# Kernel optimization log

Hardware: AMD Instinct MI355X
Metric: run time of the kernel (lower is better)

## Reference

```python
import jax, jax.numpy as jnp
import numpy as np

B, S, D, H, DFF = 4, 2048, 768, 12, 3072
DK = D // H

def setup_inputs() -> dict:
    key = jax.random.key(0)
    ks = jax.random.split(key, 16)
    sc = 0.02
    inp = {
        'src': jax.random.normal(ks[0], (B, S, D), jnp.float32),
        'mask': jnp.ones((B, 1, 1, S), jnp.int32),
        'Wq': jax.random.normal(ks[1], (D, D), jnp.float32) * sc,
        'bq': jnp.zeros((D,), jnp.float32),
        'Wk': jax.random.normal(ks[2], (D, D), jnp.float32) * sc,
        'bk': jnp.zeros((D,), jnp.float32),
        'Wv': jax.random.normal(ks[3], (D, D), jnp.float32) * sc,
        'bv': jnp.zeros((D,), jnp.float32),
        'Wo': jax.random.normal(ks[4], (D, D), jnp.float32) * sc,
        'bo': jnp.zeros((D,), jnp.float32),
        'W1': jax.random.normal(ks[5], (D, DFF), jnp.float32) * sc,
        'b1': jnp.zeros((DFF,), jnp.float32),
        'W2': jax.random.normal(ks[6], (DFF, D), jnp.float32) * sc,
        'b2': jnp.zeros((D,), jnp.float32),
        'ln1_g': jnp.ones((D,), jnp.float32), 'ln1_b': jnp.zeros((D,), jnp.float32),
        'ln2_g': jnp.ones((D,), jnp.float32), 'ln2_b': jnp.zeros((D,), jnp.float32),
    }
    return inp

def _layernorm(x, g, b, eps=1e-5):
    mu = jnp.mean(x, axis=-1, keepdims=True)
    var = jnp.mean(jnp.square(x - mu), axis=-1, keepdims=True)
    return (x - mu) * jax.lax.rsqrt(var + eps) * g + b

def reference(src, mask, Wq, bq, Wk, bk, Wv, bv, Wo, bo, W1, b1, W2, b2, ln1_g, ln1_b, ln2_g, ln2_b):
    # Multi-head self-attention (dropout in eval mode -> identity)
    q = (src @ Wq + bq).reshape(B, S, H, DK).transpose(0, 2, 1, 3)  # [B,H,S,dk]
    k = (src @ Wk + bk).reshape(B, S, H, DK).transpose(0, 2, 1, 3)
    v = (src @ Wv + bv).reshape(B, S, H, DK).transpose(0, 2, 1, 3)
    scores = jnp.einsum('bhqd,bhkd->bhqk', q, k) / jnp.sqrt(jnp.float32(DK))
    scores = jnp.where(mask == 0, jnp.float32(-1e9), scores)
    attn = jax.nn.softmax(scores, axis=-1)
    ctx = jnp.einsum('bhqk,bhkd->bhqd', attn, v)  # [B,H,S,dk]
    ctx = ctx.transpose(0, 2, 1, 3).reshape(B, S, D)
    attn_out = ctx @ Wo + bo
    x = _layernorm(src + attn_out, ln1_g, ln1_b)
    ffn = jax.nn.relu(x @ W1 + b1) @ W2 + b2
    return _layernorm(x + ffn, ln2_g, ln2_b)
```

## Files before the change

kernel.cpp:

```cpp
#include <hip/hip_runtime.h>
#include <hip/hip_bf16.h>
#include <stdint.h>

constexpr int BB = 4;
constexpr int SS = 2048;
constexpr int DD = 768;
constexpr int HH = 12;
constexpr int DKK = 64;
constexpr int DFF2 = 3072;
constexpr int MR = BB * SS;

typedef __attribute__((ext_vector_type(4))) short short4v;
typedef __attribute__((ext_vector_type(8))) short short8v;
typedef __attribute__((ext_vector_type(4))) float f32x4;
typedef __attribute__((ext_vector_type(16))) float f32x16;
typedef __attribute__((ext_vector_type(4))) float float4v;
typedef __attribute__((ext_vector_type(4))) unsigned int u32x4;

static __device__ inline short f2bs(float f) {
    __hip_bfloat16 h = __float2bfloat16(f);
    return (short)__builtin_bit_cast(unsigned short, h);
}
static __device__ inline float bs2f(short s) {
    __hip_bfloat16 h = __builtin_bit_cast(__hip_bfloat16, (unsigned short)s);
    return __bfloat162float(h);
}

static __device__ inline void glds16(const void* g, void* l) {
    __builtin_amdgcn_global_load_lds(
        (const __attribute__((address_space(1))) void*)g,
        (__attribute__((address_space(3))) void*)l, 16, 0, 0);
}

static __device__ inline unsigned cvtpk(float a, float b) {
    unsigned d;
    asm("v_cvt_pk_bf16_f32 %0, %1, %2" : "=v"(d) : "v"(a), "v"(b));
    return d;
}
static __device__ inline short8v pk4(unsigned a, unsigned b, unsigned c, unsigned d) {
    u32x4 w; w[0] = a; w[1] = b; w[2] = c; w[3] = d;
    return __builtin_bit_cast(short8v, w);
}

static __device__ inline void bar_vmcnt4() {
    __builtin_amdgcn_sched_barrier(0);
    asm volatile("s_waitcnt vmcnt(4)" ::: "memory");
    __builtin_amdgcn_s_barrier();
    __builtin_amdgcn_sched_barrier(0);
}
static __device__ inline void bar_vmcnt0() {
    __builtin_amdgcn_sched_barrier(0);
    asm volatile("s_waitcnt vmcnt(0)" ::: "memory");
    __builtin_amdgcn_s_barrier();
    __builtin_amdgcn_sched_barrier(0);
}

__global__ __launch_bounds__(256) void cast_f32_bf16(const float* __restrict__ in,
                                                     short* __restrict__ out, int n) {
    int i = (blockIdx.x * 256 + threadIdx.x) * 4;
    if (i < n) {
        float4v v = *(const float4v*)&in[i];
        short4v o;
        o[0] = f2bs(v[0]); o[1] = f2bs(v[1]); o[2] = f2bs(v[2]); o[3] = f2bs(v[3]);
        *(short4v*)&out[i] = o;
    }
}

__global__ __launch_bounds__(256) void transpose_cast(const float* __restrict__ W,
                                                      short* __restrict__ Wt, int K, int N) {
    __shared__ float tile[32][33];
    int n0 = blockIdx.x * 32, k0 = blockIdx.y * 32;
    int tx = threadIdx.x & 31, ty = threadIdx.x >> 5;
    #pragma unroll
    for (int i = 0; i < 32; i += 8)
        tile[ty + i][tx] = W[(size_t)(k0 + ty + i) * N + n0 + tx];
    __syncthreads();
    #pragma unroll
    for (int i = 0; i < 32; i += 8)
        Wt[(size_t)(n0 + ty + i) * K + k0 + tx] = f2bs(tile[tx][ty + i]);
}

__global__ __launch_bounds__(256) void vtrans(const short* __restrict__ V,
                                              short* __restrict__ Vt) {
    __shared__ short t[64][72];
    const int tid = threadIdx.x;
    const size_t base = (size_t)blockIdx.y * SS * DKK;
    const int s0 = blockIdx.x * 64;
    int r = tid >> 3, c = (tid & 7) * 8;
    #pragma unroll
    for (int it = 0; it < 2; it++)
        *(short8v*)&t[it * 32 + r][c] =
            *(const short8v*)&V[base + (size_t)(s0 + it * 32 + r) * DKK + c];
    __syncthreads();
    int d = tid >> 2, grp = (tid & 3) * 16;
    short8v o0, o1;
    #pragma unroll
    for (int e = 0; e < 8; e++) {
        int p0 = e, p1 = 8 + e;
        o0[e] = t[grp + (p0 & 3) + 8 * ((p0 >> 2) & 1) + 4 * (p0 >> 3)][d];
        o1[e] = t[grp + (p1 & 3) + 8 * ((p1 >> 2) & 1) + 4 * (p1 >> 3)][d];
    }
    int c0 = 2 * (tid & 3), c1 = c0 + 1;
    int p0 = c0 ^ (d & 7), p1 = c1 ^ (d & 7);
    *(short8v*)&Vt[base + (size_t)d * SS + s0 + p0 * 8] = o0;
    *(short8v*)&Vt[base + (size_t)d * SS + s0 + p1 * 8] = o1;
}

template <int EPI>
__global__ __launch_bounds__(256) void gemm_bt(
    const short* __restrict__ A, const short* __restrict__ Bt,
    int Nn, int Kn,
    const float* __restrict__ bias0, const float* __restrict__ bias1,
    const float* __restrict__ bias2,
    short* __restrict__ out0, short* __restrict__ out1, short* __restrict__ out2) {
    __shared__ alignas(16) short sA[3][128 * 32];
    __shared__ alignas(16) short sB[3][128 * 32];
    const int tid = threadIdx.x;
    const int wave = tid >> 6, lane = tid & 63;
    const int g = lane >> 4, qq = lane & 15;
    const int wm = (wave >> 1) * 64, wn = (wave & 1) * 64;

    const int gx = gridDim.x;
    const int nwg = gx * gridDim.y;
    const int wgid = blockIdx.y * gx + blockIdx.x;
    const int cpx = nwg >> 3;
    const int swz = (wgid & 7) * cpx + (wgid >> 3);
    const int bx = swz % gx, by = swz / gx;
    const int m0 = by * 128, n0 = bx * 128;

    const int e0 = wave * 512 + lane * 8;
    const int r0 = e0 >> 5, c0 = e0 & 31;

    const f32x4 zero = {0.0f, 0.0f, 0.0f, 0.0f};
    f32x4 acc[4][4];
    #pragma unroll
    for (int i = 0; i < 4; i++)
        #pragma unroll
        for (int j = 0; j < 4; j++) acc[i][j] = zero;

    const int NK = Kn >> 5;
    glds16(&A[(size_t)(m0 + r0) * Kn + c0], &sA[0][wave * 512]);
    glds16(&A[(size_t)(m0 + r0 + 64) * Kn + c0], &sA[0][wave * 512 + 2048]);
    glds16(&Bt[(size_t)(n0 + r0) * Kn + c0], &sB[0][wave * 512]);
    glds16(&Bt[(size_t)(n0 + r0 + 64) * Kn + c0], &sB[0][wave * 512 + 2048]);
    __syncthreads();

    int cur = 0, nxt = 1;
    for (int kt = 0; kt < NK; ++kt) {
        if (kt + 1 < NK) {
            const int k1 = (kt + 1) * 32;
            glds16(&A[(size_t)(m0 + r0) * Kn + k1 + c0], &sA[nxt][wave * 512]);
            glds16(&A[(size_t)(m0 + r0 + 64) * Kn + k1 + c0], &sA[nxt][wave * 512 + 2048]);
            glds16(&Bt[(size_t)(n0 + r0) * Kn + k1 + c0], &sB[nxt][wave * 512]);
            glds16(&Bt[(size_t)(n0 + r0 + 64) * Kn + k1 + c0], &sB[nxt][wave * 512 + 2048]);
            bar_vmcnt4();
        } else {
            bar_vmcnt0();
        }
        short8v af[4], bf[4];
        #pragma unroll
        for (int i = 0; i < 4; i++) {
            af[i] = *(const short8v*)&sA[cur][(wm + i * 16 + qq) * 32 + 8 * g];
            bf[i] = *(const short8v*)&sB[cur][(wn + i * 16 + qq) * 32 + 8 * g];
        }
        #pragma unroll
        for (int i = 0; i < 4; i++)
            #pragma unroll
            for (int j = 0; j < 4; j++)
                acc[i][j] = __builtin_amdgcn_mfma_f32_16x16x32_bf16(af[i], bf[j], acc[i][j], 0, 0, 0);
        cur = nxt;
        nxt = (nxt == 2) ? 0 : nxt + 1;
    }

    if (EPI == 2) {
        int which = bx / 6;
        const float* bias = (which == 0) ? bias0 : ((which == 1) ? bias1 : bias2);
        short* outp = (which == 0) ? out0 : ((which == 1) ? out1 : out2);
        float scale = (which == 0) ? 0.125f * 1.44269504088896f : 1.0f;
        #pragma unroll
        for (int i = 0; i < 4; i++)
            #pragma unroll
            for (int j = 0; j < 4; j++)
                #pragma unroll
                for (int r = 0; r < 4; r++) {
                    int row = m0 + wm + i * 16 + g * 4 + r;
                    int col = n0 - which * DD + wn + j * 16 + qq;
                    float vv = (acc[i][j][r] + bias[col]) * scale;
                    int b_ = row >> 11, s_ = row & 2047;
                    int h_ = col >> 6, d_ = col & 63;
                    if (which == 1)
                        d_ = (((d_ >> 3) ^ (s_ & 7)) << 3) | (d_ & 7);
                    outp[(((size_t)(b_ * HH + h_)) * SS + s_) * DKK + d_] = f2bs(vv);
                }
    } else {
        #pragma unroll
        for (int i = 0; i < 4; i++)
            #pragma unroll
            for (int j = 0; j < 4; j++)
                #pragma unroll
                for (int r = 0; r < 4; r++) {
                    int row = m0 + wm + i * 16 + g * 4 + r;
                    int col = n0 + wn + j * 16 + qq;
                    float vv = acc[i][j][r] + bias0[col];
                    if (EPI == 1) vv = fmaxf(vv, 0.0f);
                    out0[(size_t)row * Nn + col] = f2bs(vv);
                }
    }
}

__global__ __launch_bounds__(256) void attn_kernel(
    const short* __restrict__ Q, const short* __restrict__ Kb,
    const short* __restrict__ Vt, const int* __restrict__ mask,
    short* __restrict__ ctx) {
    __shared__ alignas(16) short sK[3][64 * 64];
    __shared__ alignas(16) short sV[3][64 * 64];
    __shared__ unsigned char smask[256];
    const int tid = threadIdx.x;
    const int wave = tid >> 6, lane = tid & 63;
    const int hi = lane >> 5, ln = lane & 31;
    constexpr int NT = SS / 64;

    int flat = blockIdx.y * gridDim.x + blockIdx.x;
    int nw = (flat & 7) * 96 + (flat >> 3);
    const int bh = nw >> 4, qb = nw & 15;
    const int b_ = bh / HH, h_ = bh % HH;
    const int q0 = qb * 128 + wave * 32;
    const size_t base = (size_t)bh * SS * DKK;

    {
        const int* mp = mask + b_ * SS + tid * 8;
        unsigned char by = 0;
        #pragma unroll
        for (int e = 0; e < 8; e++) by |= (unsigned char)((mp[e] != 0) << e);
        smask[tid] = by;
    }

    short8v qf[4];
    {
        const short* qp = &Q[base + (size_t)(q0 + ln) * DKK];
        #pragma unroll
        for (int c = 0; c < 4; c++)
            qf[c] = *(const short8v*)(qp + 16 * c + 8 * hi);
    }

    f32x16 O0, O1, Lacc;
    #pragma unroll
    for (int r = 0; r < 16; r++) { O0[r] = 0.0f; O1[r] = 0.0f; Lacc[r] = 0.0f; }
    f32x16 ZEROV;
    #pragma unroll
    for (int r = 0; r < 16; r++) ZEROV[r] = 0.0f;
    short8v ones8;
    #pragma unroll
    for (int e = 0; e < 8; e++) ones8[e] = (short)0x3F80;

    const int stgrow = wave * 8 + (lane >> 3);
    const int stgc = (lane & 7) * 8;
    const int rsz = (ln & 7) << 4;

    glds16(&Kb[base + (size_t)stgrow * DKK + stgc], &sK[0][wave * 512]);
    glds16(&Kb[base + (size_t)(stgrow + 32) * DKK + stgc], &sK[0][2048 + wave * 512]);
    glds16(&Vt[base + (size_t)stgrow * SS + stgc], &sV[0][wave * 512]);
    glds16(&Vt[base + (size_t)(stgrow + 32) * SS + stgc], &sV[0][2048 + wave * 512]);
    __syncthreads();

    int cur = 0, nxt = 1;
    for (int t = 0; t < NT; ++t) {
        const int kv0 = t * 64;
        if (t + 1 < NT) {
            const int kn = kv0 + 64;
            glds16(&Kb[base + (size_t)(kn + stgrow) * DKK + stgc], &sK[nxt][wave * 512]);
            glds16(&Kb[base + (size_t)(kn + stgrow + 32) * DKK + stgc], &sK[nxt][2048 + wave * 512]);
            glds16(&Vt[base + (size_t)stgrow * SS + kn + stgc], &sV[nxt][wave * 512]);
            glds16(&Vt[base + (size_t)(stgrow + 32) * SS + kn + stgc], &sV[nxt][2048 + wave * 512]);
            bar_vmcnt4();
        } else {
            bar_vmcnt0();
        }
        const char* kr0 = (const char*)&sK[cur][0] + ln * 128;
        const char* kr1 = kr0 + 32 * 128;
        const char* vr0 = (const char*)&sV[cur][0] + ln * 128;
        const char* vr1 = vr0 + 32 * 128;

        f32x16 s0, s1;
        __builtin_amdgcn_s_setprio(1);
        {
            int off = (16 * hi) ^ rsz;
            s0 = __builtin_amdgcn_mfma_f32_32x32x16_bf16(
                *(const short8v*)(kr0 + off), qf[0], ZEROV, 0, 0, 0);
            s1 = __builtin_amdgcn_mfma_f32_32x32x16_bf16(
                *(const short8v*)(kr1 + off), qf[0], ZEROV, 0, 0, 0);
        }
        #pragma unroll
        for (int c = 1; c < 4; c++) {
            int off = (32 * c + 16 * hi) ^ rsz;
            s0 = __builtin_amdgcn_mfma_f32_32x32x16_bf16(
                *(const short8v*)(kr0 + off), qf[c], s0, 0, 0, 0);
            s1 = __builtin_amdgcn_mfma_f32_32x32x16_bf16(
                *(const short8v*)(kr1 + off), qf[c], s1, 0, 0, 0);
        }
        __builtin_amdgcn_s_setprio(0);

        uint64_t mb = *(const uint64_t*)&smask[kv0 >> 3];
        if (mb != ~0ull) {
            #pragma unroll
            for (int r = 0; r < 16; r++) {
                int kvr = (r & 3) + 8 * (r >> 2) + 4 * hi;
                if (!((mb >> kvr) & 1)) s0[r] = -1.5e9f;
                if (!((mb >> (kvr + 32)) & 1)) s1[r] = -1.5e9f;
            }
        }

        unsigned w0[8], w1[8];
        #pragma unroll
        for (int r8 = 0; r8 < 8; ++r8) {
            float a0 = __builtin_amdgcn_exp2f(s0[2 * r8]);
            float a1 = __builtin_amdgcn_exp2f(s0[2 * r8 + 1]);
            w0[r8] = cvtpk(a0, a1);
            float b0 = __builtin_amdgcn_exp2f(s1[2 * r8]);
            float b1 = __builtin_amdgcn_exp2f(s1[2 * r8 + 1]);
            w1[r8] = cvtpk(b0, b1);
        }

        short8v p00 = pk4(w0[0], w0[1], w0[2], w0[3]);
        short8v p01 = pk4(w0[4], w0[5], w0[6], w0[7]);
        short8v p10 = pk4(w1[0], w1[1], w1[2], w1[3]);
        short8v p11 = pk4(w1[4], w1[5], w1[6], w1[7]);

        __builtin_amdgcn_s_setprio(1);
        #pragma unroll
        for (int cc = 0; cc < 4; cc++) {
            int off = (32 * cc + 16 * hi) ^ rsz;
            short8v pa = (cc == 0) ? p00 : (cc == 1) ? p01 : (cc == 2) ? p10 : p11;
            O0 = __builtin_amdgcn_mfma_f32_32x32x16_bf16(
                pa, *(const short8v*)(vr0 + off), O0, 0, 0, 0);
            O1 = __builtin_amdgcn_mfma_f32_32x32x16_bf16(
                pa, *(const short8v*)(vr1 + off), O1, 0, 0, 0);
            Lacc = __builtin_amdgcn_mfma_f32_32x32x16_bf16(pa, ones8, Lacc, 0, 0, 0);
        }
        __builtin_amdgcn_s_setprio(0);
        cur = nxt;
        nxt = (nxt == 2) ? 0 : nxt + 1;
    }

    #pragma unroll
    for (int r = 0; r < 16; r++) {
        int rho = (r & 3) + 8 * (r >> 2) + 4 * hi;
        float li = 1.0f / Lacc[r];
        size_t rowoff = (size_t)(b_ * SS + q0 + rho) * DD + h_ * DKK;
        ctx[rowoff + ln] = f2bs(O0[r] * li);
        ctx[rowoff + 32 + ln] = f2bs(O1[r] * li);
    }
}

template <int IN1BF, int WB, int WF>
__global__ __launch_bounds__(256) void ln_fused(
    const void* __restrict__ in1v, const short* __restrict__ in2,
    const float* __restrict__ gw, const float* __restrict__ bw,
    short* __restrict__ outb, float* __restrict__ outf) {
    const int row = blockIdx.x;
    const int tid = threadIdx.x;
    float4v v = {0.0f, 0.0f, 0.0f, 0.0f};
    if (tid < 192) {
        short4v b = *(const short4v*)&in2[(size_t)row * DD + tid * 4];
        if (IN1BF) {
            short4v a = *(const short4v*)&((const short*)in1v)[(size_t)row * DD + tid * 4];
            #pragma unroll
            for (int e = 0; e < 4; e++) v[e] = bs2f(a[e]) + bs2f(b[e]);
        } else {
            float4v a = *(const float4v*)&((const float*)in1v)[(size_t)row * DD + tid * 4];
            #pragma unroll
            for (int e = 0; e < 4; e++) v[e] = a[e] + bs2f(b[e]);
        }
    }
    float s = v[0] + v[1] + v[2] + v[3];
    float s2 = v[0] * v[0] + v[1] * v[1] + v[2] * v[2] + v[3] * v[3];
    #pragma unroll
    for (int off = 1; off < 64; off <<= 1) {
        s += __shfl_xor(s, off);
        s2 += __shfl_xor(s2, off);
    }
    __shared__ float red[8];
    int wv = tid >> 6;
    if ((tid & 63) == 0) { red[wv] = s; red[4 + wv] = s2; }
    __syncthreads();
    s = red[0] + red[1] + red[2] + red[3];
    s2 = red[4] + red[5] + red[6] + red[7];
    float mu = s / DD;
    float var = s2 / DD - mu * mu;
    float rs = rsqrtf(var + 1e-5f);
    if (tid < 192) {
        float4v gv = *(const float4v*)&gw[tid * 4];
        float4v bv = *(const float4v*)&bw[tid * 4];
        float4v y;
        #pragma unroll
        for (int e = 0; e < 4; e++) y[e] = (v[e] - mu) * rs * gv[e] + bv[e];
        if (WB) {
            short4v o;
            #pragma unroll
            for (int e = 0; e < 4; e++) o[e] = f2bs(y[e]);
            *(short4v*)&outb[(size_t)row * DD + tid * 4] = o;
        }
        if (WF) *(float4v*)&outf[(size_t)row * DD + tid * 4] = y;
    }
}

extern "C" void kernel_launch(void* const* d_in, const int* in_sizes, int n_in,
                              void* d_out, int out_size, void* d_ws, size_t ws_size,
                              hipStream_t stream) {
    (void)in_sizes; (void)n_in; (void)out_size; (void)ws_size;
    const float* src = (const float*)d_in[0];
    const int* mask = (const int*)d_in[1];
    const float* Wq = (const float*)d_in[2];
    const float* bq = (const float*)d_in[3];
    const float* Wk = (const float*)d_in[4];
    const float* bk = (const float*)d_in[5];
    const float* Wv = (const float*)d_in[6];
    const float* bv = (const float*)d_in[7];
    const float* Wo = (const float*)d_in[8];
    const float* bo = (const float*)d_in[9];
    const float* W1 = (const float*)d_in[10];
    const float* b1 = (const float*)d_in[11];
    const float* W2 = (const float*)d_in[12];
    const float* b2 = (const float*)d_in[13];
    const float* ln1_g = (const float*)d_in[14];
    const float* ln1_b = (const float*)d_in[15];
    const float* ln2_g = (const float*)d_in[16];
    const float* ln2_b = (const float*)d_in[17];

    char* ws = (char*)d_ws;
    const size_t SB = (size_t)MR * DD * 2;
    short* src_b  = (short*)(ws);
    short* Wqkv_t = (short*)(ws + SB);
    short* qb     = (short*)(ws + SB + 3538944);
    short* kb_    = qb + (size_t)MR * DD;
    short* vb_    = kb_ + (size_t)MR * DD;
    short* ctxb   = vb_ + (size_t)MR * DD;
    short* hb     = qb;
    short* Wo_t   = (short*)(ws + SB + 3538944 + 4 * SB);
    short* x_b    = (short*)(ws + SB + 3538944 + 4 * SB + 1179648);
    short* W1_t   = (short*)((char*)x_b + SB);
    short* W2_t   = (short*)((char*)W1_t + 4718592);
    short* vt_    = x_b;
    short* attn_b = src_b;
    short* ffn_b  = src_b;

    cast_f32_bf16<<<(MR * DD) / 1024, 256, 0, stream>>>(src, src_b, MR * DD);
    transpose_cast<<<dim3(24, 24), 256, 0, stream>>>(Wq, Wqkv_t, DD, DD);
    transpose_cast<<<dim3(24, 24), 256, 0, stream>>>(Wk, Wqkv_t + DD * DD, DD, DD);
    transpose_cast<<<dim3(24, 24), 256, 0, stream>>>(Wv, Wqkv_t + 2 * DD * DD, DD, DD);
    transpose_cast<<<dim3(24, 24), 256, 0, stream>>>(Wo, Wo_t, DD, DD);
    transpose_cast<<<dim3(96, 24), 256, 0, stream>>>(W1, W1_t, DD, DFF2);
    transpose_cast<<<dim3(24, 96), 256, 0, stream>>>(W2, W2_t, DFF2, DD);

    gemm_bt<2><<<dim3(2304 / 128, MR / 128), 256, 0, stream>>>(
        src_b, Wqkv_t, 2304, DD, bq, bk, bv, qb, kb_, vb_);

    vtrans<<<dim3(SS / 64, BB * HH), 256, 0, stream>>>(vb_, vt_);

    attn_kernel<<<dim3(SS / 128, BB * HH), 256, 0, stream>>>(qb, kb_, vt_, mask, ctxb);

    gemm_bt<0><<<dim3(DD / 128, MR / 128), 256, 0, stream>>>(
        ctxb, Wo_t, DD, DD, bo, nullptr, nullptr, attn_b, nullptr, nullptr);

    ln_fused<0, 1, 0><<<MR, 256, 0, stream>>>(src, attn_b, ln1_g, ln1_b, x_b, nullptr);

    gemm_bt<1><<<dim3(DFF2 / 128, MR / 128), 256, 0, stream>>>(
        x_b, W1_t, DFF2, DD, b1, nullptr, nullptr, hb, nullptr, nullptr);
    gemm_bt<0><<<dim3(DD / 128, MR / 128), 256, 0, stream>>>(
        hb, W2_t, DD, DFF2, b2, nullptr, nullptr, ffn_b, nullptr, nullptr);

    ln_fused<1, 0, 1><<<MR, 256, 0, stream>>>(x_b, ffn_b, ln2_g, ln2_b, nullptr, (float*)d_out);
}
```

Baseline: 316.3 us.

## Use 64-wide N tiles for D-output GEMMs and restructure attention pipeline

Templates the GEMM on the N tile width and launches the two 768-wide output GEMMs (Wo, W2) with 64-column tiles, doubling their workgroup count to fill more compute units. The attention kernel moves from a 3-stage to a 2-stage K/V buffer that prefetches two tiles ahead and refills the current buffer after a barrier. It also replaces the MFMA-based row-sum (multiply by a ones vector) with a scalar accumulation of the exponentials plus a cross-lane shuffle and a shared-memory lookup. The smaller tiles lower per-block data reuse, and the extra barrier per iteration may cost some overlap.

```diff
diff --git a/kernel.cpp b/kernel.cpp
--- a/kernel.cpp
+++ b/kernel.cpp
@@ -48,9 +48,20 @@
     __builtin_amdgcn_s_barrier();
     __builtin_amdgcn_sched_barrier(0);
 }
+static __device__ inline void bar_vmcnt3() {
+    __builtin_amdgcn_sched_barrier(0);
+    asm volatile("s_waitcnt vmcnt(3)" ::: "memory");
+    __builtin_amdgcn_s_barrier();
+    __builtin_amdgcn_sched_barrier(0);
+}
 static __device__ inline void bar_vmcnt0() {
     __builtin_amdgcn_sched_barrier(0);
     asm volatile("s_waitcnt vmcnt(0)" ::: "memory");
+    __builtin_amdgcn_s_barrier();
+    __builtin_amdgcn_sched_barrier(0);
+}
+static __device__ inline void bar_plain() {
+    __builtin_amdgcn_sched_barrier(0);
     __builtin_amdgcn_s_barrier();
     __builtin_amdgcn_sched_barrier(0);
 }
@@ -106,19 +117,20 @@
     *(short8v*)&Vt[base + (size_t)d * SS + s0 + p1 * 8] = o1;
 }
 
-template <int EPI>
+template <int EPI, int BN>
 __global__ __launch_bounds__(256) void gemm_bt(
     const short* __restrict__ A, const short* __restrict__ Bt,
     int Nn, int Kn,
     const float* __restrict__ bias0, const float* __restrict__ bias1,
     const float* __restrict__ bias2,
     short* __restrict__ out0, short* __restrict__ out1, short* __restrict__ out2) {
+    constexpr int NJ = BN / 32;
     __shared__ alignas(16) short sA[3][128 * 32];
-    __shared__ alignas(16) short sB[3][128 * 32];
+    __shared__ alignas(16) short sB[3][BN * 32];
     const int tid = threadIdx.x;
     const int wave = tid >> 6, lane = tid & 63;
     const int g = lane >> 4, qq = lane & 15;
-    const int wm = (wave >> 1) * 64, wn = (wave & 1) * 64;
+    const int wm = (wave >> 1) * 64, wn = (wave & 1) * (BN / 2);
 
     const int gx = gridDim.x;
     const int nwg = gx * gridDim.y;
@@ -126,23 +138,24 @@
     const int cpx = nwg >> 3;
     const int swz = (wgid & 7) * cpx + (wgid >> 3);
     const int bx = swz % gx, by = swz / gx;
-    const int m0 = by * 128, n0 = bx * 128;
+    const int m0 = by * 128, n0 = bx * BN;
 
     const int e0 = wave * 512 + lane * 8;
     const int r0 = e0 >> 5, c0 = e0 & 31;
 
     const f32x4 zero = {0.0f, 0.0f, 0.0f, 0.0f};
-    f32x4 acc[4][4];
+    f32x4 acc[4][NJ];
     #pragma unroll
     for (int i = 0; i < 4; i++)
         #pragma unroll
-        for (int j = 0; j < 4; j++) acc[i][j] = zero;
+        for (int j = 0; j < NJ; j++) acc[i][j] = zero;
 
     const int NK = Kn >> 5;
     glds16(&A[(size_t)(m0 + r0) * Kn + c0], &sA[0][wave * 512]);
     glds16(&A[(size_t)(m0 + r0 + 64) * Kn + c0], &sA[0][wave * 512 + 2048]);
     glds16(&Bt[(size_t)(n0 + r0) * Kn + c0], &sB[0][wave * 512]);
-    glds16(&Bt[(size_t)(n0 + r0 + 64) * Kn + c0], &sB[0][wave * 512 + 2048]);
+    if constexpr (BN == 128)
+        glds16(&Bt[(size_t)(n0 + r0 + 64) * Kn + c0], &sB[0][wave * 512 + 2048]);
     __syncthreads();
 
     int cur = 0, nxt = 1;
@@ -152,27 +165,29 @@
             glds16(&A[(size_t)(m0 + r0) * Kn + k1 + c0], &sA[nxt][wave * 512]);
             glds16(&A[(size_t)(m0 + r0 + 64) * Kn + k1 + c0], &sA[nxt][wave * 512 + 2048]);
             glds16(&Bt[(size_t)(n0 + r0) * Kn + k1 + c0], &sB[nxt][wave * 512]);
-            glds16(&Bt[(size_t)(n0 + r0 + 64) * Kn + k1 + c0], &sB[nxt][wave * 512 + 2048]);
-            bar_vmcnt4();
+            if constexpr (BN == 128)
+                glds16(&Bt[(size_t)(n0 + r0 + 64) * Kn + k1 + c0], &sB[nxt][wave * 512 + 2048]);
+            if constexpr (BN == 128) bar_vmcnt4(); else bar_vmcnt3();
         } else {
             bar_vmcnt0();
         }
-        short8v af[4], bf[4];
-        #pragma unroll
-        for (int i = 0; i < 4; i++) {
+        short8v af[4], bf[NJ];
+        #pragma unroll
+        for (int i = 0; i < 4; i++)
             af[i] = *(const short8v*)&sA[cur][(wm + i * 16 + qq) * 32 + 8 * g];
-            bf[i] = *(const short8v*)&sB[cur][(wn + i * 16 + qq) * 32 + 8 * g];
-        }
+        #pragma unroll
+        for (int j = 0; j < NJ; j++)
+            bf[j] = *(const short8v*)&sB[cur][(wn + j * 16 + qq) * 32 + 8 * g];
         #pragma unroll
         for (int i = 0; i < 4; i++)
             #pragma unroll
-            for (int j = 0; j < 4; j++)
+            for (int j = 0; j < NJ; j++)
                 acc[i][j] = __builtin_amdgcn_mfma_f32_16x16x32_bf16(af[i], bf[j], acc[i][j], 0, 0, 0);
         cur = nxt;
         nxt = (nxt == 2) ? 0 : nxt + 1;
     }
 
-    if (EPI == 2) {
+    if constexpr (EPI == 2) {
         int which = bx / 6;
         const float* bias = (which == 0) ? bias0 : ((which == 1) ? bias1 : bias2);
         short* outp = (which == 0) ? out0 : ((which == 1) ? out1 : out2);
@@ -180,7 +195,7 @@
         #pragma unroll
         for (int i = 0; i < 4; i++)
             #pragma unroll
-            for (int j = 0; j < 4; j++)
+            for (int j = 0; j < NJ; j++)
                 #pragma unroll
                 for (int r = 0; r < 4; r++) {
                     int row = m0 + wm + i * 16 + g * 4 + r;
@@ -196,7 +211,7 @@
         #pragma unroll
         for (int i = 0; i < 4; i++)
             #pragma unroll
-            for (int j = 0; j < 4; j++)
+            for (int j = 0; j < NJ; j++)
                 #pragma unroll
                 for (int r = 0; r < 4; r++) {
                     int row = m0 + wm + i * 16 + g * 4 + r;
@@ -212,8 +227,9 @@
     const short* __restrict__ Q, const short* __restrict__ Kb,
     const short* __restrict__ Vt, const int* __restrict__ mask,
     short* __restrict__ ctx) {
-    __shared__ alignas(16) short sK[3][64 * 64];
-    __shared__ alignas(16) short sV[3][64 * 64];
+    __shared__ alignas(16) short sK[2][64 * 64];
+    __shared__ alignas(16) short sV[2][64 * 64];
+    __shared__ float sAl[4][32];
     __shared__ unsigned char smask[256];
     const int tid = threadIdx.x;
     const int wave = tid >> 6, lane = tid & 63;
@@ -243,15 +259,10 @@
             qf[c] = *(const short8v*)(qp + 16 * c + 8 * hi);
     }
 
-    f32x16 O0, O1, Lacc;
-    #pragma unroll
-    for (int r = 0; r < 16; r++) { O0[r] = 0.0f; O1[r] = 0.0f; Lacc[r] = 0.0f; }
-    f32x16 ZEROV;
-    #pragma unroll
-    for (int r = 0; r < 16; r++) ZEROV[r] = 0.0f;
-    short8v ones8;
-    #pragma unroll
-    for (int e = 0; e < 8; e++) ones8[e] = (short)0x3F80;
+    f32x16 O0, O1, ZEROV;
+    #pragma unroll
+    for (int r = 0; r < 16; r++) { O0[r] = 0.0f; O1[r] = 0.0f; ZEROV[r] = 0.0f; }
+    float lreg = 0.0f;
 
     const int stgrow = wave * 8 + (lane >> 3);
     const int stgc = (lane & 7) * 8;
@@ -261,20 +272,18 @@
     glds16(&Kb[base + (size_t)(stgrow + 32) * DKK + stgc], &sK[0][2048 + wave * 512]);
     glds16(&Vt[base + (size_t)stgrow * SS + stgc], &sV[0][wave * 512]);
     glds16(&Vt[base + (size_t)(stgrow + 32) * SS + stgc], &sV[0][2048 + wave * 512]);
+    glds16(&Kb[base + (size_t)(64 + stgrow) * DKK + stgc], &sK[1][wave * 512]);
+    glds16(&Kb[base + (size_t)(64 + stgrow + 32) * DKK + stgc], &sK[1][2048 + wave * 512]);
+    glds16(&Vt[base + (size_t)stgrow * SS + 64 + stgc], &sV[1][wave * 512]);
+    glds16(&Vt[base + (size_t)(stgrow + 32) * SS + 64 + stgc], &sV[1][2048 + wave * 512]);
     __syncthreads();
 
-    int cur = 0, nxt = 1;
     for (int t = 0; t < NT; ++t) {
         const int kv0 = t * 64;
-        if (t + 1 < NT) {
-            const int kn = kv0 + 64;
-            glds16(&Kb[base + (size_t)(kn + stgrow) * DKK + stgc], &sK[nxt][wave * 512]);
-            glds16(&Kb[base + (size_t)(kn + stgrow + 32) * DKK + stgc], &sK[nxt][2048 + wave * 512]);
-            glds16(&Vt[base + (size_t)stgrow * SS + kn + stgc], &sV[nxt][wave * 512]);
-            glds16(&Vt[base + (size_t)(stgrow + 32) * SS + kn + stgc], &sV[nxt][2048 + wave * 512]);
-            bar_vmcnt4();
-        } else {
-            bar_vmcnt0();
+        const int cur = t & 1;
+        if (t) {
+            if (t + 1 < NT) bar_vmcnt4();
+            else bar_vmcnt0();
         }
         const char* kr0 = (const char*)&sK[cur][0] + ln * 128;
         const char* kr1 = kr0 + 32 * 128;
@@ -310,16 +319,20 @@
             }
         }
 
+        float ps = 0.0f;
         unsigned w0[8], w1[8];
         #pragma unroll
         for (int r8 = 0; r8 < 8; ++r8) {
             float a0 = __builtin_amdgcn_exp2f(s0[2 * r8]);
             float a1 = __builtin_amdgcn_exp2f(s0[2 * r8 + 1]);
+            ps += a0 + a1;
             w0[r8] = cvtpk(a0, a1);
             float b0 = __builtin_amdgcn_exp2f(s1[2 * r8]);
             float b1 = __builtin_amdgcn_exp2f(s1[2 * r8 + 1]);
+            ps += b0 + b1;
             w1[r8] = cvtpk(b0, b1);
         }
+        lreg += ps;
 
         short8v p00 = pk4(w0[0], w0[1], w0[2], w0[3]);
         short8v p01 = pk4(w0[4], w0[5], w0[6], w0[7]);
@@ -335,17 +348,25 @@
                 pa, *(const short8v*)(vr0 + off), O0, 0, 0, 0);
             O1 = __builtin_amdgcn_mfma_f32_32x32x16_bf16(
                 pa, *(const short8v*)(vr1 + off), O1, 0, 0, 0);
-            Lacc = __builtin_amdgcn_mfma_f32_32x32x16_bf16(pa, ones8, Lacc, 0, 0, 0);
         }
         __builtin_amdgcn_s_setprio(0);
-        cur = nxt;
-        nxt = (nxt == 2) ? 0 : nxt + 1;
-    }
-
+
+        bar_plain();
+        if (t + 2 < NT) {
+            const int kn = kv0 + 128;
+            glds16(&Kb[base + (size_t)(kn + stgrow) * DKK + stgc], &sK[cur][wave * 512]);
+            glds16(&Kb[base + (size_t)(kn + stgrow + 32) * DKK + stgc], &sK[cur][2048 + wave * 512]);
+            glds16(&Vt[base + (size_t)stgrow * SS + kn + stgc], &sV[cur][wave * 512]);
+            glds16(&Vt[base + (size_t)(stgrow + 32) * SS + kn + stgc], &sV[cur][2048 + wave * 512]);
+        }
+    }
+
+    lreg += __shfl_xor(lreg, 32);
+    sAl[wave][ln] = 1.0f / lreg;
     #pragma unroll
     for (int r = 0; r < 16; r++) {
         int rho = (r & 3) + 8 * (r >> 2) + 4 * hi;
-        float li = 1.0f / Lacc[r];
+        float li = sAl[wave][rho];
         size_t rowoff = (size_t)(b_ * SS + q0 + rho) * DD + h_ * DKK;
         ctx[rowoff + ln] = f2bs(O0[r] * li);
         ctx[rowoff + 32 + ln] = f2bs(O1[r] * li);
@@ -452,21 +473,21 @@
     transpose_cast<<<dim3(96, 24), 256, 0, stream>>>(W1, W1_t, DD, DFF2);
     transpose_cast<<<dim3(24, 96), 256, 0, stream>>>(W2, W2_t, DFF2, DD);
 
-    gemm_bt<2><<<dim3(2304 / 128, MR / 128), 256, 0, stream>>>(
+    gemm_bt<2, 128><<<dim3(2304 / 128, MR / 128), 256, 0, stream>>>(
         src_b, Wqkv_t, 2304, DD, bq, bk, bv, qb, kb_, vb_);
 
     vtrans<<<dim3(SS / 64, BB * HH), 256, 0, stream>>>(vb_, vt_);
 
     attn_kernel<<<dim3(SS / 128, BB * HH), 256, 0, stream>>>(qb, kb_, vt_, mask, ctxb);
 
-    gemm_bt<0><<<dim3(DD / 128, MR / 128), 256, 0, stream>>>(
+    gemm_bt<0, 64><<<dim3(DD / 64, MR / 128), 256, 0, stream>>>(
         ctxb, Wo_t, DD, DD, bo, nullptr, nullptr, attn_b, nullptr, nullptr);
 
     ln_fused<0, 1, 0><<<MR, 256, 0, stream>>>(src, attn_b, ln1_g, ln1_b, x_b, nullptr);
 
-    gemm_bt<1><<<dim3(DFF2 / 128, MR / 128), 256, 0, stream>>>(
+    gemm_bt<1, 128><<<dim3(DFF2 / 128, MR / 128), 256, 0, stream>>>(
         x_b, W1_t, DFF2, DD, b1, nullptr, nullptr, hb, nullptr, nullptr);
-    gemm_bt<0><<<dim3(DD / 128, MR / 128), 256, 0, stream>>>(
+    gemm_bt<0, 64><<<dim3(DD / 64, MR / 128), 256, 0, stream>>>(
         hb, W2_t, DD, DFF2, b2, nullptr, nullptr, ffn_b, nullptr, nullptr);
 
     ln_fused<1, 0, 1><<<MR, 256, 0, stream>>>(x_b, ffn_b, ln2_g, ln2_b, nullptr, (float*)d_out);
```

After: 318.2 us. About the same (+0.6%).
